# Performance work log

Measured on AMD Instinct MI355X. Metric: run time of the kernel, lower is better.

## Reference

```python
import jax, jax.numpy as jnp
import numpy as np

N_NODES = 100000
D_IN = 128
H_DIM = 128
N_EDGES = 1600000


def _gcn_conv(x, src, dst, dinv, W, b):
    # PyG GCNConv(improved=True): h = x @ W; out = A_hat h + b,
    # A_hat = D^{-1/2} (A + 2I) D^{-1/2}
    h = x @ W                                   # [N, H]
    norm = dinv[src] * dinv[dst]                # [E]
    agg = jnp.zeros_like(h).at[dst].add(h[src] * norm[:, None])
    agg = agg + h * (2.0 * dinv * dinv)[:, None]  # self-loop, weight 2.0
    return agg + b


def setup_inputs() -> dict:
    key = jax.random.key(0)
    ks = jax.random.split(key, 12)
    s = 1.0 / np.sqrt(D_IN)
    sh = 1.0 / np.sqrt(2 * H_DIM)
    inp = {
        "x": jax.random.normal(ks[0], (N_NODES, D_IN), jnp.float32),
        "edge_index": jax.random.randint(ks[1], (2, N_EDGES), 0, N_NODES, jnp.int64),
        # GCNConv weights (in -> hidden), bias
        "Wz": jax.random.uniform(ks[2], (D_IN, H_DIM), jnp.float32, -s, s),
        "bz": jnp.zeros((H_DIM,), jnp.float32),
        "Wr": jax.random.uniform(ks[3], (D_IN, H_DIM), jnp.float32, -s, s),
        "br": jnp.zeros((H_DIM,), jnp.float32),
        "Wh": jax.random.uniform(ks[4], (D_IN, H_DIM), jnp.float32, -s, s),
        "bh": jnp.zeros((H_DIM,), jnp.float32),
        # TGCN gate linears: Linear(2h, h)
        "lzW": jax.random.uniform(ks[5], (2 * H_DIM, H_DIM), jnp.float32, -sh, sh),
        "lzb": jax.random.uniform(ks[6], (H_DIM,), jnp.float32, -sh, sh),
        "lrW": jax.random.uniform(ks[7], (2 * H_DIM, H_DIM), jnp.float32, -sh, sh),
        "lrb": jax.random.uniform(ks[8], (H_DIM,), jnp.float32, -sh, sh),
        "lhW": jax.random.uniform(ks[9], (2 * H_DIM, H_DIM), jnp.float32, -sh, sh),
        "lhb": jax.random.uniform(ks[10], (H_DIM,), jnp.float32, -sh, sh),
        # final linear2: hidden -> 1
        "W2": jax.random.uniform(ks[11], (H_DIM, 1), jnp.float32, -1 / np.sqrt(H_DIM), 1 / np.sqrt(H_DIM)),
        "b2": jnp.zeros((1,), jnp.float32),
    }
    return inp


def reference(x, edge_index, Wz, bz, Wr, br, Wh, bh, lzW, lzb, lrW, lrb, lhW, lhb, W2, b2):
    src, dst = edge_index[0], edge_index[1]
    n = x.shape[0]
    # improved GCN norm: deg includes self-loop weight 2
    deg = jnp.zeros((n,), x.dtype).at[dst].add(jnp.ones_like(src, x.dtype)) + 2.0
    dinv = jnp.where(deg > 0, deg ** -0.5, 0.0)
    # TGCN cell with H0 = 0
    H0 = jnp.zeros((n, Wz.shape[1]), x.dtype)
    Z = jax.nn.sigmoid(jnp.concatenate([_gcn_conv(x, src, dst, dinv, Wz, bz), H0], axis=1) @ lzW + lzb)
    R = jax.nn.sigmoid(jnp.concatenate([_gcn_conv(x, src, dst, dinv, Wr, br), H0], axis=1) @ lrW + lrb)
    Ht = jnp.tanh(jnp.concatenate([_gcn_conv(x, src, dst, dinv, Wh, bh), H0 * R], axis=1) @ lhW + lhb)
    H = Z * H0 + (1.0 - Z) * Ht
    # forward: relu output is discarded (y = h overwrites), then linear2
    return H @ W2 + b2
```

## Files before the change

kernel.cpp:

```cpp
#include <hip/hip_runtime.h>
#include <math.h>

#define D 128
#define BSHIFT 9
#define CAP 12288

typedef __attribute__((ext_vector_type(8))) short s8v;
typedef __attribute__((ext_vector_type(8))) unsigned short us8;
typedef __attribute__((ext_vector_type(4))) unsigned short us4;
typedef __attribute__((ext_vector_type(4))) float f4v;

__device__ __forceinline__ float bf2f(unsigned short u) {
    union { unsigned int i; float f; } v; v.i = ((unsigned int)u) << 16; return v.f;
}
__device__ __forceinline__ unsigned short f2bf(float f) {
    union { float f; unsigned int i; } v; v.f = f;
    unsigned int r = v.i + 0x7FFFu + ((v.i >> 16) & 1u);
    return (unsigned short)(r >> 16);
}

__global__ __launch_bounds__(256) void k_part1(const int* __restrict__ src,
                                               const int* __restrict__ dst, int E,
                                               int* __restrict__ bcur,
                                               unsigned long long* __restrict__ pairs) {
    __shared__ int cnt[256];
    __shared__ int base[256];
    int tid = threadIdx.x;
    int chunk = (E + gridDim.x - 1) / gridDim.x;
    int e0 = blockIdx.x * chunk;
    int e1 = min(E, e0 + chunk);
    cnt[tid] = 0;
    __syncthreads();
    for (int e = e0 + tid; e < e1; e += 256)
        atomicAdd(&cnt[dst[e] >> BSHIFT], 1);
    __syncthreads();
    if (cnt[tid] > 0) base[tid] = tid * CAP + atomicAdd(&bcur[tid], cnt[tid]);
    __syncthreads();
    cnt[tid] = 0;
    __syncthreads();
    for (int e = e0 + tid; e < e1; e += 256) {
        int d = dst[e];
        int bk = d >> BSHIFT;
        int r = atomicAdd(&cnt[bk], 1);
        pairs[base[bk] + r] = ((unsigned long long)(unsigned int)d << 32) | (unsigned int)src[e];
    }
}

__global__ void k_bscan(const int* __restrict__ bcur, int NB, int* __restrict__ bbase) {
    __shared__ int ts[256];
    int t = threadIdx.x;
    int v = (t < NB) ? bcur[t] : 0;
    ts[t] = v; __syncthreads();
    for (int off = 1; off < 256; off <<= 1) {
        int add = (t >= off) ? ts[t - off] : 0;
        __syncthreads();
        ts[t] += add;
        __syncthreads();
    }
    if (t < NB) bbase[t] = ts[t] - v;
}

__global__ __launch_bounds__(256) void k_part2(const unsigned long long* __restrict__ pairs,
                                               const int* __restrict__ bcur,
                                               const int* __restrict__ bbase,
                                               int N, int E,
                                               int* __restrict__ rowptr,
                                               float* __restrict__ dinv,
                                               int* __restrict__ esrc) {
    __shared__ int cnt[512];
    __shared__ int lcur[512];
    __shared__ int ts[256];
    int b = blockIdx.x, tid = threadIdx.x;
    int n0 = b << BSHIFT;
    int nn = min(N - n0, 1 << BSHIFT);
    int tot = bcur[b];
    long pbase = (long)b * CAP;
    int obase = bbase[b];

    cnt[tid] = 0; cnt[tid + 256] = 0;
    __syncthreads();
    for (int i = tid; i < tot; i += 256)
        atomicAdd(&cnt[(int)(pairs[pbase + i] >> 32) - n0], 1);
    __syncthreads();

    int a0 = cnt[2 * tid], a1 = cnt[2 * tid + 1];
    int s = a0 + a1;
    ts[tid] = s; __syncthreads();
    for (int off = 1; off < 256; off <<= 1) {
        int add = (tid >= off) ? ts[tid - off] : 0;
        __syncthreads();
        ts[tid] += add;
        __syncthreads();
    }
    int excl = ts[tid] - s;
    lcur[2 * tid]     = obase + excl;
    lcur[2 * tid + 1] = obase + excl + a0;
    if (2 * tid < nn) {
        rowptr[n0 + 2 * tid] = obase + excl;
        dinv[n0 + 2 * tid]   = rsqrtf((float)a0 + 2.0f);
    }
    if (2 * tid + 1 < nn) {
        rowptr[n0 + 2 * tid + 1] = obase + excl + a0;
        dinv[n0 + 2 * tid + 1]   = rsqrtf((float)a1 + 2.0f);
    }
    if (b == 0 && tid == 0) rowptr[N] = E;
    __syncthreads();

    for (int i = tid; i < tot; i += 256) {
        unsigned long long p = pairs[pbase + i];
        int dl = (int)(p >> 32) - n0;
        int pos = atomicAdd(&lcur[dl], 1);
        esrc[pos] = (int)(p & 0xffffffffu);
    }
}

__global__ void k_xcast(const float* __restrict__ x, unsigned short* __restrict__ xb, int n4) {
    int i = blockIdx.x * blockDim.x + threadIdx.x;
    if (i >= n4) return;
    float4 v = ((const float4*)x)[i];
    us4 o;
    o[0] = f2bf(v.x); o[1] = f2bf(v.y); o[2] = f2bf(v.z); o[3] = f2bf(v.w);
    ((us4*)xb)[i] = o;
}

__global__ __launch_bounds__(256) void k_gather(const unsigned short* __restrict__ xb,
                                                const int* __restrict__ esrc,
                                                const int* __restrict__ rowptr,
                                                const float* __restrict__ dinv,
                                                unsigned short* __restrict__ xab, int N) {
    int node = (blockIdx.x * blockDim.x + threadIdx.x) >> 5;
    int sub  = threadIdx.x & 31;
    if (node >= N) return;
    int eo = sub >> 4, cs = sub & 15;
    int start = rowptr[node], end = rowptr[node + 1];
    float dd = dinv[node];
    float acc[8];
    #pragma unroll
    for (int j = 0; j < 8; ++j) acc[j] = 0.f;

    for (int base = start; base < end; base += 32) {
        int cnt = min(32, end - base);
        int myedge = 0; float mynorm = 0.f;
        if (sub < cnt) { myedge = esrc[base + sub]; mynorm = dinv[myedge]; }
        int pairs = (cnt + 1) >> 1;
        int i = 0;
        for (; i + 3 < pairs; i += 4) {
            int i0 = 2 * i + eo;
            int   s0 = __shfl(myedge, i0,     32); float w0 = __shfl(mynorm, i0,     32);
            int   s1 = __shfl(myedge, i0 + 2, 32); float w1 = __shfl(mynorm, i0 + 2, 32);
            int   s2 = __shfl(myedge, i0 + 4, 32); float w2 = __shfl(mynorm, i0 + 4, 32);
            int   s3 = __shfl(myedge, i0 + 6, 32); float w3 = __shfl(mynorm, i0 + 6, 32);
            us8 v0 = *(const us8*)(xb + (size_t)s0 * D + cs * 8);
            us8 v1 = *(const us8*)(xb + (size_t)s1 * D + cs * 8);
            us8 v2 = *(const us8*)(xb + (size_t)s2 * D + cs * 8);
            us8 v3 = *(const us8*)(xb + (size_t)s3 * D + cs * 8);
            #pragma unroll
            for (int j = 0; j < 8; ++j) acc[j] += bf2f(v0[j]) * w0;
            #pragma unroll
            for (int j = 0; j < 8; ++j) acc[j] += bf2f(v1[j]) * w1;
            #pragma unroll
            for (int j = 0; j < 8; ++j) acc[j] += bf2f(v2[j]) * w2;
            #pragma unroll
            for (int j = 0; j < 8; ++j) acc[j] += bf2f(v3[j]) * w3;
        }
        for (; i < pairs; ++i) {
            int i0 = 2 * i + eo;
            int   s0 = __shfl(myedge, i0, 32); float w0 = __shfl(mynorm, i0, 32);
            us8 v0 = *(const us8*)(xb + (size_t)s0 * D + cs * 8);
            #pragma unroll
            for (int j = 0; j < 8; ++j) acc[j] += bf2f(v0[j]) * w0;
        }
    }
    #pragma unroll
    for (int j = 0; j < 8; ++j) acc[j] += __shfl_xor(acc[j], 16);
    if (eo == 0) {
        us8 xs = *(const us8*)(xb + (size_t)node * D + cs * 8);
        float sfac = 2.f * dd * dd;
        us8 r;
        #pragma unroll
        for (int j = 0; j < 8; ++j) r[j] = f2bf(acc[j] * dd + bf2f(xs[j]) * sfac);
        *(us8*)(xab + (size_t)node * D + cs * 8) = r;
    }
}

__global__ void k_prep(const float* __restrict__ Wz, const float* __restrict__ bz,
                       const float* __restrict__ lzW, const float* __restrict__ lzb,
                       const float* __restrict__ Wh, const float* __restrict__ bh,
                       const float* __restrict__ lhW, const float* __restrict__ lhb,
                       unsigned short* __restrict__ Mt, float* __restrict__ c) {
    int j = threadIdx.x;
    int k = blockIdx.x;
    int jj = j & 127;
    const float* W = (j < 128) ? Wz : Wh;
    const float* L = (j < 128) ? lzW : lhW;
    float s = 0.f;
    for (int t = 0; t < 128; ++t) s += W[k * 128 + t] * L[t * 128 + jj];
    Mt[(size_t)j * 128 + k] = f2bf(s);
    if (k == 0) {
        const float* b  = (j < 128) ? bz  : bh;
        const float* lb = (j < 128) ? lzb : lhb;
        float cs = lb[jj];
        for (int t = 0; t < 128; ++t) cs += b[t] * L[t * 128 + jj];
        c[j] = cs;
    }
}

#define ASTRIDE 136
__global__ __launch_bounds__(256, 4) void k_ep_mfma(
    const unsigned short* __restrict__ xab, const unsigned short* __restrict__ Mt,
    const float* __restrict__ c, const float* __restrict__ W2,
    const float* __restrict__ b2, float* __restrict__ out, int N) {
    __shared__ unsigned short Ast[64 * ASTRIDE];
    __shared__ float pbuf[4][64];

    int tid = threadIdx.x;
    int n0 = blockIdx.x * 64;
    int wv = tid >> 6;
    int lane = tid & 63;
    int l = lane & 15, q = lane >> 4;

    #pragma unroll
    for (int j = 0; j < 4; ++j) {
        int idx = tid + 256 * j;
        int row = idx >> 4, c16 = idx & 15;
        us8 v = {0, 0, 0, 0, 0, 0, 0, 0};
        if (n0 + row < N) v = *(const us8*)(xab + (size_t)(n0 + row) * D + c16 * 8);
        *(us8*)&Ast[row * ASTRIDE + c16 * 8] = v;
    }
    __syncthreads();

    int tz0 = 2 * wv;
    f4v acc[4][4];
    #pragma unroll
    for (int i = 0; i < 4; ++i)
        #pragma unroll
        for (int nt = 0; nt < 4; ++nt) acc[i][nt] = (f4v){0.f, 0.f, 0.f, 0.f};

    const unsigned short* Bb = Mt + (size_t)l * 128 + q * 8;

    #pragma unroll
    for (int ks = 0; ks < 4; ++ks) {
        s8v b[4];
        #pragma unroll
        for (int i = 0; i < 2; ++i) {
            b[i]     = *(const s8v*)(Bb + (size_t)(tz0 + i) * 16 * 128 + ks * 32);
            b[2 + i] = *(const s8v*)(Bb + (size_t)(8 + tz0 + i) * 16 * 128 + ks * 32);
        }
        #pragma unroll
        for (int nt = 0; nt < 4; ++nt) {
            s8v a = *(const s8v*)&Ast[(nt * 16 + l) * ASTRIDE + ks * 32 + q * 8];
            #pragma unroll
            for (int i = 0; i < 4; ++i)
                acc[i][nt] = __builtin_amdgcn_mfma_f32_16x16x32_bf16(a, b[i], acc[i][nt], 0, 0, 0);
        }
    }

    float p[4][4];
    #pragma unroll
    for (int nt = 0; nt < 4; ++nt)
        #pragma unroll
        for (int r = 0; r < 4; ++r) p[nt][r] = 0.f;
    #pragma unroll
    for (int i = 0; i < 2; ++i) {
        int col = (tz0 + i) * 16 + l;
        float cz = c[col], ch = c[128 + col], w2 = W2[col];
        #pragma unroll
        for (int nt = 0; nt < 4; ++nt)
            #pragma unroll
            for (int r = 0; r < 4; ++r) {
                float gz = acc[i][nt][r] + cz;
                float gh = acc[2 + i][nt][r] + ch;
                float z  = 1.f / (1.f + __expf(-gz));
                float ht = 1.f - 2.f / (__expf(2.f * gh) + 1.f);
                p[nt][r] += (1.f - z) * ht * w2;
            }
    }
    #pragma unroll
    for (int nt = 0; nt < 4; ++nt)
        #pragma unroll
        for (int r = 0; r < 4; ++r) {
            p[nt][r] += __shfl_xor(p[nt][r], 1);
            p[nt][r] += __shfl_xor(p[nt][r], 2);
            p[nt][r] += __shfl_xor(p[nt][r], 4);
            p[nt][r] += __shfl_xor(p[nt][r], 8);
        }
    if (l == 0) {
        #pragma unroll
        for (int nt = 0; nt < 4; ++nt)
            #pragma unroll
            for (int r = 0; r < 4; ++r)
                pbuf[wv][nt * 16 + q * 4 + r] = p[nt][r];
    }
    __syncthreads();
    if (tid < 64) {
        int n = n0 + tid;
        if (n < N)
            out[n] = pbuf[0][tid] + pbuf[1][tid] + pbuf[2][tid] + pbuf[3][tid] + b2[0];
    }
}

extern "C" void kernel_launch(void* const* d_in, const int* in_sizes, int n_in,
                              void* d_out, int out_size, void* d_ws, size_t ws_size,
                              hipStream_t stream) {
    const float* x    = (const float*)d_in[0];
    const int*   eidx = (const int*)d_in[1];
    const float* Wz   = (const float*)d_in[2];
    const float* bz   = (const float*)d_in[3];
    const float* Wh   = (const float*)d_in[6];
    const float* bh   = (const float*)d_in[7];
    const float* lzW  = (const float*)d_in[8];
    const float* lzb  = (const float*)d_in[9];
    const float* lhW  = (const float*)d_in[12];
    const float* lhb  = (const float*)d_in[13];
    const float* W2   = (const float*)d_in[14];
    const float* b2   = (const float*)d_in[15];
    float* out = (float*)d_out;

    int N = in_sizes[0] / D;
    int E = in_sizes[1] / 2;
    const int* src = eidx;
    const int* dst = eidx + E;
    int NB = (N + (1 << BSHIFT) - 1) >> BSHIFT;

    char* ws = (char*)d_ws;
    size_t off = 0;
    auto alloc = [&](size_t bytes) { void* p = ws + off; off += (bytes + 511) & ~(size_t)511; return p; };
    unsigned short* xb   = (unsigned short*)alloc((size_t)N * D * 2);
    unsigned short* xab  = (unsigned short*)alloc((size_t)N * D * 2);
    int*   rowptr = (int*)  alloc((size_t)(N + 1) * 4);
    float* dinv   = (float*)alloc((size_t)N * 4);
    int*   esrc   = (int*)  alloc((size_t)E * 4);
    int*   bcur   = (int*)  alloc(256 * 4);
    int*   bbase  = (int*)  alloc(256 * 4);
    unsigned short* Mt = (unsigned short*)alloc(256 * 128 * 2);
    float* c      = (float*)alloc(256 * 4);
    unsigned long long* pairs = (unsigned long long*)xab;

    hipMemsetAsync(bcur, 0, 256 * sizeof(int), stream);

    k_part1<<<512, 256, 0, stream>>>(src, dst, E, bcur, pairs);
    k_bscan<<<1, 256, 0, stream>>>(bcur, NB, bbase);
    k_part2<<<NB, 256, 0, stream>>>(pairs, bcur, bbase, N, E, rowptr, dinv, esrc);
    k_xcast<<<(N * (D / 4) + 255) / 256, 256, 0, stream>>>(x, xb, N * (D / 4));
    k_gather<<<(N * 32 + 255) / 256, 256, 0, stream>>>(xb, esrc, rowptr, dinv, xab, N);
    k_prep<<<128, 256, 0, stream>>>(Wz, bz, lzW, lzb, Wh, bh, lhW, lhb, Mt, c);
    k_ep_mfma<<<(N + 63) / 64, 256, 0, stream>>>(xab, Mt, c, W2, b2, out, N);
}
```

Measured before the change: 271.2 us.

## Fuse gather into MFMA epilogue and merge partition, cast, and prep kernels

Merges the edge-partition pass, the x-to-bf16 cast and the weight-prep matmul into one launch, split by block index. The bucket prefix scan moves into k_part2 as a per-block reduction. The neighbour gather is folded into the MFMA epilogue kernel, which writes aggregated rows straight into shared memory, so the xab intermediate is never written to or read back from global memory. Four kernel launches go away as well. In exchange, the fused gather/epilogue kernel runs the gather with launch bounds set for 4 blocks, and each half-wave now processes 8 nodes in turn, which may cut memory-level parallelism during the gather.

After: 249.6 us. 8.0% less time.

```diff
diff --git a/kernel.cpp b/kernel.cpp
--- a/kernel.cpp
+++ b/kernel.cpp
@@ -4,6 +4,9 @@
 #define D 128
 #define BSHIFT 9
 #define CAP 12288
+#define EPT 13
+#define P1B 481
+#define XCB 12500
 
 typedef __attribute__((ext_vector_type(8))) short s8v;
 typedef __attribute__((ext_vector_type(8))) unsigned short us8;
@@ -19,51 +22,74 @@
     return (unsigned short)(r >> 16);
 }
 
-__global__ __launch_bounds__(256) void k_part1(const int* __restrict__ src,
-                                               const int* __restrict__ dst, int E,
-                                               int* __restrict__ bcur,
-                                               unsigned long long* __restrict__ pairs) {
+__global__ __launch_bounds__(256) void k_combo(
+    const int* __restrict__ src, const int* __restrict__ dst, int E,
+    int* __restrict__ bcur, unsigned long long* __restrict__ pairs,
+    const float* __restrict__ x, unsigned short* __restrict__ xb, int n4,
+    const float* __restrict__ Wz, const float* __restrict__ bz,
+    const float* __restrict__ lzW, const float* __restrict__ lzb,
+    const float* __restrict__ Wh, const float* __restrict__ bh,
+    const float* __restrict__ lhW, const float* __restrict__ lhb,
+    unsigned short* __restrict__ Mt, float* __restrict__ c) {
     __shared__ int cnt[256];
     __shared__ int base[256];
-    int tid = threadIdx.x;
-    int chunk = (E + gridDim.x - 1) / gridDim.x;
-    int e0 = blockIdx.x * chunk;
-    int e1 = min(E, e0 + chunk);
-    cnt[tid] = 0;
-    __syncthreads();
-    for (int e = e0 + tid; e < e1; e += 256)
-        atomicAdd(&cnt[dst[e] >> BSHIFT], 1);
-    __syncthreads();
-    if (cnt[tid] > 0) base[tid] = tid * CAP + atomicAdd(&bcur[tid], cnt[tid]);
-    __syncthreads();
-    cnt[tid] = 0;
-    __syncthreads();
-    for (int e = e0 + tid; e < e1; e += 256) {
-        int d = dst[e];
-        int bk = d >> BSHIFT;
-        int r = atomicAdd(&cnt[bk], 1);
-        pairs[base[bk] + r] = ((unsigned long long)(unsigned int)d << 32) | (unsigned int)src[e];
-    }
-}
-
-__global__ void k_bscan(const int* __restrict__ bcur, int NB, int* __restrict__ bbase) {
-    __shared__ int ts[256];
-    int t = threadIdx.x;
-    int v = (t < NB) ? bcur[t] : 0;
-    ts[t] = v; __syncthreads();
-    for (int off = 1; off < 256; off <<= 1) {
-        int add = (t >= off) ? ts[t - off] : 0;
-        __syncthreads();
-        ts[t] += add;
-        __syncthreads();
-    }
-    if (t < NB) bbase[t] = ts[t] - v;
+    int bx = blockIdx.x, tid = threadIdx.x;
+
+    if (bx < P1B) {
+        int ed[EPT], es[EPT], rk[EPT];
+        int e0 = bx * (EPT * 256) + tid;
+        cnt[tid] = 0;
+        __syncthreads();
+        #pragma unroll
+        for (int i = 0; i < EPT; ++i) {
+            int e = e0 + i * 256;
+            bool ok = e < E;
+            ed[i] = ok ? dst[e] : 0;
+            es[i] = ok ? src[e] : 0;
+            rk[i] = ok ? atomicAdd(&cnt[ed[i] >> BSHIFT], 1) : 0;
+        }
+        __syncthreads();
+        if (cnt[tid] > 0) base[tid] = tid * CAP + atomicAdd(&bcur[tid], cnt[tid]);
+        __syncthreads();
+        #pragma unroll
+        for (int i = 0; i < EPT; ++i) {
+            int e = e0 + i * 256;
+            if (e < E) {
+                int bk = ed[i] >> BSHIFT;
+                pairs[base[bk] + rk[i]] =
+                    ((unsigned long long)(unsigned int)ed[i] << 32) | (unsigned int)es[i];
+            }
+        }
+    } else if (bx < P1B + XCB) {
+        int i = (bx - P1B) * 256 + tid;
+        if (i < n4) {
+            float4 v = ((const float4*)x)[i];
+            us4 o;
+            o[0] = f2bf(v.x); o[1] = f2bf(v.y); o[2] = f2bf(v.z); o[3] = f2bf(v.w);
+            ((us4*)xb)[i] = o;
+        }
+    } else {
+        int k = bx - (P1B + XCB);
+        int j = tid;
+        int jj = j & 127;
+        const float* W = (j < 128) ? Wz : Wh;
+        const float* L = (j < 128) ? lzW : lhW;
+        float s = 0.f;
+        for (int t = 0; t < 128; ++t) s += W[k * 128 + t] * L[t * 128 + jj];
+        Mt[(size_t)j * 128 + k] = f2bf(s);
+        if (k == 0) {
+            const float* b  = (j < 128) ? bz  : bh;
+            const float* lb = (j < 128) ? lzb : lhb;
+            float cs = lb[jj];
+            for (int t = 0; t < 128; ++t) cs += b[t] * L[t * 128 + jj];
+            c[j] = cs;
+        }
+    }
 }
 
 __global__ __launch_bounds__(256) void k_part2(const unsigned long long* __restrict__ pairs,
                                                const int* __restrict__ bcur,
-                                               const int* __restrict__ bbase,
-                                               int N, int E,
+                                               int NB, int N, int E,
                                                int* __restrict__ rowptr,
                                                float* __restrict__ dinv,
                                                int* __restrict__ esrc) {
@@ -75,7 +101,15 @@
     int nn = min(N - n0, 1 << BSHIFT);
     int tot = bcur[b];
     long pbase = (long)b * CAP;
-    int obase = bbase[b];
+
+    ts[tid] = (tid < b) ? bcur[tid] : 0;
+    __syncthreads();
+    for (int off = 128; off > 0; off >>= 1) {
+        if (tid < off) ts[tid] += ts[tid + off];
+        __syncthreads();
+    }
+    int obase = ts[0];
+    __syncthreads();
 
     cnt[tid] = 0; cnt[tid + 256] = 0;
     __syncthreads();
@@ -114,100 +148,13 @@
     }
 }
 
-__global__ void k_xcast(const float* __restrict__ x, unsigned short* __restrict__ xb, int n4) {
-    int i = blockIdx.x * blockDim.x + threadIdx.x;
-    if (i >= n4) return;
-    float4 v = ((const float4*)x)[i];
-    us4 o;
-    o[0] = f2bf(v.x); o[1] = f2bf(v.y); o[2] = f2bf(v.z); o[3] = f2bf(v.w);
-    ((us4*)xb)[i] = o;
-}
-
-__global__ __launch_bounds__(256) void k_gather(const unsigned short* __restrict__ xb,
-                                                const int* __restrict__ esrc,
-                                                const int* __restrict__ rowptr,
-                                                const float* __restrict__ dinv,
-                                                unsigned short* __restrict__ xab, int N) {
-    int node = (blockIdx.x * blockDim.x + threadIdx.x) >> 5;
-    int sub  = threadIdx.x & 31;
-    if (node >= N) return;
-    int eo = sub >> 4, cs = sub & 15;
-    int start = rowptr[node], end = rowptr[node + 1];
-    float dd = dinv[node];
-    float acc[8];
-    #pragma unroll
-    for (int j = 0; j < 8; ++j) acc[j] = 0.f;
-
-    for (int base = start; base < end; base += 32) {
-        int cnt = min(32, end - base);
-        int myedge = 0; float mynorm = 0.f;
-        if (sub < cnt) { myedge = esrc[base + sub]; mynorm = dinv[myedge]; }
-        int pairs = (cnt + 1) >> 1;
-        int i = 0;
-        for (; i + 3 < pairs; i += 4) {
-            int i0 = 2 * i + eo;
-            int   s0 = __shfl(myedge, i0,     32); float w0 = __shfl(mynorm, i0,     32);
-            int   s1 = __shfl(myedge, i0 + 2, 32); float w1 = __shfl(mynorm, i0 + 2, 32);
-            int   s2 = __shfl(myedge, i0 + 4, 32); float w2 = __shfl(mynorm, i0 + 4, 32);
-            int   s3 = __shfl(myedge, i0 + 6, 32); float w3 = __shfl(mynorm, i0 + 6, 32);
-            us8 v0 = *(const us8*)(xb + (size_t)s0 * D + cs * 8);
-            us8 v1 = *(const us8*)(xb + (size_t)s1 * D + cs * 8);
-            us8 v2 = *(const us8*)(xb + (size_t)s2 * D + cs * 8);
-            us8 v3 = *(const us8*)(xb + (size_t)s3 * D + cs * 8);
-            #pragma unroll
-            for (int j = 0; j < 8; ++j) acc[j] += bf2f(v0[j]) * w0;
-            #pragma unroll
-            for (int j = 0; j < 8; ++j) acc[j] += bf2f(v1[j]) * w1;
-            #pragma unroll
-            for (int j = 0; j < 8; ++j) acc[j] += bf2f(v2[j]) * w2;
-            #pragma unroll
-            for (int j = 0; j < 8; ++j) acc[j] += bf2f(v3[j]) * w3;
-        }
-        for (; i < pairs; ++i) {
-            int i0 = 2 * i + eo;
-            int   s0 = __shfl(myedge, i0, 32); float w0 = __shfl(mynorm, i0, 32);
-            us8 v0 = *(const us8*)(xb + (size_t)s0 * D + cs * 8);
-            #pragma unroll
-            for (int j = 0; j < 8; ++j) acc[j] += bf2f(v0[j]) * w0;
-        }
-    }
-    #pragma unroll
-    for (int j = 0; j < 8; ++j) acc[j] += __shfl_xor(acc[j], 16);
-    if (eo == 0) {
-        us8 xs = *(const us8*)(xb + (size_t)node * D + cs * 8);
-        float sfac = 2.f * dd * dd;
-        us8 r;
-        #pragma unroll
-        for (int j = 0; j < 8; ++j) r[j] = f2bf(acc[j] * dd + bf2f(xs[j]) * sfac);
-        *(us8*)(xab + (size_t)node * D + cs * 8) = r;
-    }
-}
-
-__global__ void k_prep(const float* __restrict__ Wz, const float* __restrict__ bz,
-                       const float* __restrict__ lzW, const float* __restrict__ lzb,
-                       const float* __restrict__ Wh, const float* __restrict__ bh,
-                       const float* __restrict__ lhW, const float* __restrict__ lhb,
-                       unsigned short* __restrict__ Mt, float* __restrict__ c) {
-    int j = threadIdx.x;
-    int k = blockIdx.x;
-    int jj = j & 127;
-    const float* W = (j < 128) ? Wz : Wh;
-    const float* L = (j < 128) ? lzW : lhW;
-    float s = 0.f;
-    for (int t = 0; t < 128; ++t) s += W[k * 128 + t] * L[t * 128 + jj];
-    Mt[(size_t)j * 128 + k] = f2bf(s);
-    if (k == 0) {
-        const float* b  = (j < 128) ? bz  : bh;
-        const float* lb = (j < 128) ? lzb : lhb;
-        float cs = lb[jj];
-        for (int t = 0; t < 128; ++t) cs += b[t] * L[t * 128 + jj];
-        c[j] = cs;
-    }
-}
-
 #define ASTRIDE 136
-__global__ __launch_bounds__(256, 4) void k_ep_mfma(
-    const unsigned short* __restrict__ xab, const unsigned short* __restrict__ Mt,
+__global__ __launch_bounds__(256, 4) void k_gather_ep(
+    const unsigned short* __restrict__ xb,
+    const int* __restrict__ esrc,
+    const int* __restrict__ rowptr,
+    const float* __restrict__ dinv,
+    const unsigned short* __restrict__ Mt,
     const float* __restrict__ c, const float* __restrict__ W2,
     const float* __restrict__ b2, float* __restrict__ out, int N) {
     __shared__ unsigned short Ast[64 * ASTRIDE];
@@ -215,20 +162,72 @@
 
     int tid = threadIdx.x;
     int n0 = blockIdx.x * 64;
+    int hw = tid >> 5;
+    int sub = tid & 31;
+    int eo = sub >> 4, cs = sub & 15;
+
+    for (int rep = 0; rep < 8; ++rep) {
+        int node = n0 + rep * 8 + hw;
+        int row = rep * 8 + hw;
+        if (node < N) {
+            int start = rowptr[node], end = rowptr[node + 1];
+            float dd = dinv[node];
+            float acc[8];
+            #pragma unroll
+            for (int j = 0; j < 8; ++j) acc[j] = 0.f;
+            for (int base = start; base < end; base += 32) {
+                int cntv = min(32, end - base);
+                int myedge = 0; float mynorm = 0.f;
+                if (sub < cntv) { myedge = esrc[base + sub]; mynorm = dinv[myedge]; }
+                int pr = (cntv + 1) >> 1;
+                int i = 0;
+                for (; i + 3 < pr; i += 4) {
+                    int i0 = 2 * i + eo;
+                    int   s0 = __shfl(myedge, i0,     32); float w0 = __shfl(mynorm, i0,     32);
+                    int   s1 = __shfl(myedge, i0 + 2, 32); float w1 = __shfl(mynorm, i0 + 2, 32);
+                    int   s2 = __shfl(myedge, i0 + 4, 32); float w2 = __shfl(mynorm, i0 + 4, 32);
+                    int   s3 = __shfl(myedge, i0 + 6, 32); float w3 = __shfl(mynorm, i0 + 6, 32);
+                    us8 v0 = *(const us8*)(xb + (size_t)s0 * D + cs * 8);
+                    us8 v1 = *(const us8*)(xb + (size_t)s1 * D + cs * 8);
+                    us8 v2 = *(const us8*)(xb + (size_t)s2 * D + cs * 8);
+                    us8 v3 = *(const us8*)(xb + (size_t)s3 * D + cs * 8);
+                    #pragma unroll
+                    for (int j = 0; j < 8; ++j) acc[j] += bf2f(v0[j]) * w0;
+                    #pragma unroll
+                    for (int j = 0; j < 8; ++j) acc[j] += bf2f(v1[j]) * w1;
+                    #pragma unroll
+                    for (int j = 0; j < 8; ++j) acc[j] += bf2f(v2[j]) * w2;
+                    #pragma unroll
+                    for (int j = 0; j < 8; ++j) acc[j] += bf2f(v3[j]) * w3;
+                }
+                for (; i < pr; ++i) {
+                    int i0 = 2 * i + eo;
+                    int   s0 = __shfl(myedge, i0, 32); float w0 = __shfl(mynorm, i0, 32);
+                    us8 v0 = *(const us8*)(xb + (size_t)s0 * D + cs * 8);
+                    #pragma unroll
+                    for (int j = 0; j < 8; ++j) acc[j] += bf2f(v0[j]) * w0;
+                }
+            }
+            #pragma unroll
+            for (int j = 0; j < 8; ++j) acc[j] += __shfl_xor(acc[j], 16);
+            if (eo == 0) {
+                us8 xs = *(const us8*)(xb + (size_t)node * D + cs * 8);
+                float sfac = 2.f * dd * dd;
+                us8 r;
+                #pragma unroll
+                for (int j = 0; j < 8; ++j) r[j] = f2bf(acc[j] * dd + bf2f(xs[j]) * sfac);
+                *(us8*)&Ast[row * ASTRIDE + cs * 8] = r;
+            }
+        } else if (eo == 0) {
+            us8 z = {0, 0, 0, 0, 0, 0, 0, 0};
+            *(us8*)&Ast[row * ASTRIDE + cs * 8] = z;
+        }
+    }
+    __syncthreads();
+
     int wv = tid >> 6;
     int lane = tid & 63;
     int l = lane & 15, q = lane >> 4;
-
-    #pragma unroll
-    for (int j = 0; j < 4; ++j) {
-        int idx = tid + 256 * j;
-        int row = idx >> 4, c16 = idx & 15;
-        us8 v = {0, 0, 0, 0, 0, 0, 0, 0};
-        if (n0 + row < N) v = *(const us8*)(xab + (size_t)(n0 + row) * D + c16 * 8);
-        *(us8*)&Ast[row * ASTRIDE + c16 * 8] = v;
-    }
-    __syncthreads();
-
     int tz0 = 2 * wv;
     f4v acc[4][4];
     #pragma unroll
@@ -325,24 +324,22 @@
     char* ws = (char*)d_ws;
     size_t off = 0;
     auto alloc = [&](size_t bytes) { void* p = ws + off; off += (bytes + 511) & ~(size_t)511; return p; };
-    unsigned short* xb   = (unsigned short*)alloc((size_t)N * D * 2);
-    unsigned short* xab  = (unsigned short*)alloc((size_t)N * D * 2);
+    unsigned short* xb = (unsigned short*)alloc((size_t)N * D * 2);
+    unsigned long long* pairs = (unsigned long long*)alloc((size_t)NB * CAP * 8);
     int*   rowptr = (int*)  alloc((size_t)(N + 1) * 4);
     float* dinv   = (float*)alloc((size_t)N * 4);
     int*   esrc   = (int*)  alloc((size_t)E * 4);
     int*   bcur   = (int*)  alloc(256 * 4);
-    int*   bbase  = (int*)  alloc(256 * 4);
     unsigned short* Mt = (unsigned short*)alloc(256 * 128 * 2);
     float* c      = (float*)alloc(256 * 4);
-    unsigned long long* pairs = (unsigned long long*)xab;
 
     hipMemsetAsync(bcur, 0, 256 * sizeof(int), stream);
 
-    k_part1<<<512, 256, 0, stream>>>(src, dst, E, bcur, pairs);
-    k_bscan<<<1, 256, 0, stream>>>(bcur, NB, bbase);
-    k_part2<<<NB, 256, 0, stream>>>(pairs, bcur, bbase, N, E, rowptr, dinv, esrc);
-    k_xcast<<<(N * (D / 4) + 255) / 256, 256, 0, stream>>>(x, xb, N * (D / 4));
-    k_gather<<<(N * 32 + 255) / 256, 256, 0, stream>>>(xb, esrc, rowptr, dinv, xab, N);
-    k_prep<<<128, 256, 0, stream>>>(Wz, bz, lzW, lzb, Wh, bh, lhW, lhb, Mt, c);
-    k_ep_mfma<<<(N + 63) / 64, 256, 0, stream>>>(xab, Mt, c, W2, b2, out, N);
-}
+    int n4 = N * (D / 4);
+    k_combo<<<P1B + XCB + 128, 256, 0, stream>>>(
+        src, dst, E, bcur, pairs, x, xb, n4,
+        Wz, bz, lzW, lzb, Wh, bh, lhW, lhb, Mt, c);
+    k_part2<<<NB, 256, 0, stream>>>(pairs, bcur, NB, N, E, rowptr, dinv, esrc);
+    k_gather_ep<<<(N + 63) / 64, 256, 0, stream>>>(
+        xb, esrc, rowptr, dinv, Mt, c, W2, b2, out, N);
+}
```
